# Kernel optimization log

Measured on AMD Instinct MI355X. Metric: run time of the kernel, lower is better.

Reference implementation:

```python
import jax, jax.numpy as jnp
import numpy as np

B, N, NODE_DIM = 64, 64, 192
H = 256          # node_hidden_dim
PDIM = 64        # property_embedding_dim
NUM_EDGE_TYPE = 5
T = 4            # message-passing rounds
E = 16384        # total edges (flattened batched graph)
E_SEL = 65536    # selected candidate pairs


def setup_inputs() -> dict:
    key = jax.random.key(0)
    ks = jax.random.split(key, 24)
    def g(k, shape, scale=0.05):
        return jax.random.normal(k, shape, dtype=jnp.float32) * scale
    inp = {
        "x": jax.random.normal(ks[0], (B, N, NODE_DIM), dtype=jnp.float32),
        "edge_index": jax.random.randint(ks[1], (2, E), 0, B * N, dtype=jnp.int32),
        "edge_attr": jax.random.uniform(ks[2], (E, NUM_EDGE_TYPE), dtype=jnp.float32),
        "props": jax.random.normal(ks[3], (B, 1), dtype=jnp.float32),
        "sel_b": jax.random.randint(ks[4], (E_SEL,), 0, B, dtype=jnp.int32),
        "sel_i": jax.random.randint(ks[5], (E_SEL,), 0, N, dtype=jnp.int32),
        "sel_j": jax.random.randint(ks[6], (E_SEL,), 0, N, dtype=jnp.int32),
        "golden_edge": jax.random.randint(ks[7], (E_SEL,), 0, NUM_EDGE_TYPE, dtype=jnp.int32),
        # parameters
        "W_prop": g(ks[8], (1, PDIM)), "b_prop": jnp.zeros((PDIM,), jnp.float32),
        "W_in": g(ks[9], (NODE_DIM, H)), "b_in": jnp.zeros((H,), jnp.float32),
        "W_msg": g(ks[10], (H + NUM_EDGE_TYPE, H)), "b_msg": jnp.zeros((H,), jnp.float32),
        "W_upd": g(ks[11], (2 * H, H)), "b_upd": jnp.zeros((H,), jnp.float32),
        "W_add": g(ks[12], (H + PDIM, H)), "b_add": jnp.zeros((H,), jnp.float32),
        "W1": g(ks[13], (2 * H, H)), "b1": jnp.zeros((H,), jnp.float32),
        "W2": g(ks[14], (H, H)), "b2": jnp.zeros((H,), jnp.float32),
        "W3": g(ks[15], (H, 2 * H)), "b3": jnp.zeros((2 * H,), jnp.float32),
        "W_out": g(ks[16], (2 * H, NUM_EDGE_TYPE)), "b_out": jnp.zeros((NUM_EDGE_TYPE,), jnp.float32),
    }
    return inp


def reference(x, edge_index, edge_attr, props, sel_b, sel_i, sel_j, golden_edge,
              W_prop, b_prop, W_in, b_in, W_msg, b_msg, W_upd, b_upd,
              W_add, b_add, W1, b1, W2, b2, W3, b3, W_out, b_out):
    BN = B * N
    node_x = x.reshape(BN, NODE_DIM)
    src, dst = edge_index[0], edge_index[1]

    # --- GNN node embedding (t rounds of message passing, opaque Encoder.embed_node) ---
    h = jax.nn.relu(node_x @ W_in + b_in)                       # [BN, H]
    for _ in range(T):
        msg_in = jnp.concatenate([h[src], edge_attr], axis=-1)  # [E, H+num_edge_type]
        msg = jax.nn.relu(msg_in @ W_msg + b_msg)               # [E, H]
        agg = jax.ops.segment_sum(msg, dst, num_segments=BN)    # [BN, H]
        h = jax.nn.relu(jnp.concatenate([h, agg], axis=-1) @ W_upd + b_upd)

    node_emb = h.reshape(B, N, H)

    # --- property conditioning + addition linear ---
    prop = props @ W_prop + b_prop                               # [B, PDIM]
    propp = jnp.broadcast_to(prop[:, None, :], (B, N, PDIM))
    node_embg = jnp.concatenate([node_emb, propp], axis=-1) @ W_add + b_add  # [B, N, H]

    # --- gather selected (src, dst) pairs directly (equiv. to repeat_interleave + boolean mask) ---
    flat = node_embg.reshape(BN, H)
    src_e = flat[sel_b * N + sel_i]                              # [E_SEL, H]
    dst_e = flat[sel_b * N + sel_j]                              # [E_SEL, H]
    pair = jnp.concatenate([src_e, dst_e], axis=-1)              # [E_SEL, 2H]

    # --- edge predictor MLP (3 layers, ReLU between) + output linear ---
    h1 = jax.nn.relu(pair @ W1 + b1)
    h2 = jax.nn.relu(h1 @ W2 + b2)
    h3 = h2 @ W3 + b3
    logits = h3 @ W_out + b_out                                  # [E_SEL, num_edge_type]

    # --- cross entropy (mean) ---
    logp = jax.nn.log_softmax(logits, axis=-1)
    loss = -jnp.mean(jnp.take_along_axis(logp, golden_edge[:, None].astype(jnp.int32), axis=-1))
    return loss
```

## Files before the change

kernel.cpp:

```cpp
#include <hip/hip_runtime.h>
#include <math.h>

#define BN 4096
#define N_PER_B 64
#define NE 16384
#define NSEL 65536
#define NET 5
#define PD 64
#define H1STR 260
#define FSTR 264
#define PTILES 4

typedef float f32x4 __attribute__((ext_vector_type(4)));
typedef float f32x16 __attribute__((ext_vector_type(16)));
typedef short short8 __attribute__((ext_vector_type(8)));
typedef short short4v __attribute__((ext_vector_type(4)));

__device__ __forceinline__ unsigned short f2bf(float f) {
    unsigned int u = __builtin_bit_cast(unsigned int, f);
    u += 0x7fff + ((u >> 16) & 1);
    return (unsigned short)(u >> 16);
}
__device__ __forceinline__ float bf_lo(unsigned int u) {
    return __builtin_bit_cast(float, u << 16);
}
__device__ __forceinline__ float bf_hi(unsigned int u) {
    return __builtin_bit_cast(float, u & 0xffff0000u);
}
__device__ __forceinline__ unsigned int pack2(float a, float b) {
    return (unsigned)f2bf(a) | ((unsigned)f2bf(b) << 16);
}
__device__ __forceinline__ short8 ld_frag(const unsigned short* p) {
    const short4v lo = *(const short4v*)(p);
    const short4v hi = *(const short4v*)(p + 4);
    return __builtin_shufflevector(lo, hi, 0, 1, 2, 3, 4, 5, 6, 7);
}
__device__ __forceinline__ unsigned int addrelu2(unsigned int a, unsigned int b, unsigned int c) {
    const float lo = fmaxf(bf_lo(a) + bf_lo(b) + bf_lo(c), 0.f);
    const float hi = fmaxf(bf_hi(a) + bf_hi(b) + bf_hi(c), 0.f);
    return pack2(lo, hi);
}

__global__ __launch_bounds__(256) void k_hist(const int* __restrict__ eidx,
                                              int* __restrict__ deg)
{
    const int e = blockIdx.x * 256 + threadIdx.x;
    atomicAdd(&deg[eidx[NE + e]], 1);
}

__global__ __launch_bounds__(256) void csr_scan(const int* __restrict__ deg,
                                                int* __restrict__ row_start,
                                                int* __restrict__ cursor)
{
    __shared__ int sums[256];
    const int tid = threadIdx.x;
    const int base = tid * 16;
    int local[16];
    int s = 0;
    #pragma unroll
    for (int i = 0; i < 16; ++i) { local[i] = s; s += deg[base + i]; }
    sums[tid] = s;
    __syncthreads();
    for (int off = 1; off < 256; off <<= 1) {
        const int v = sums[tid];
        const int add = (tid >= off) ? sums[tid - off] : 0;
        __syncthreads();
        sums[tid] = v + add;
        __syncthreads();
    }
    const int offset = (tid == 0) ? 0 : sums[tid - 1];
    #pragma unroll
    for (int i = 0; i < 16; ++i) {
        const int v = offset + local[i];
        row_start[base + i] = v;
        cursor[base + i] = v;
    }
    if (tid == 255) row_start[4096] = NE;
}

__global__ __launch_bounds__(256) void csr_scatter(const int* __restrict__ eidx,
                                                   int* __restrict__ cursor,
                                                   int* __restrict__ srcs,
                                                   int* __restrict__ epos)
{
    const int e = blockIdx.x * 256 + threadIdx.x;
    const int pos = atomicAdd(&cursor[eidx[NE + e]], 1);
    srcs[pos] = eidx[e];
    epos[e] = pos;
}

__global__ __launch_bounds__(256) void k_pre(
    const float* __restrict__ W_in, const float* __restrict__ W_msg,
    const float* __restrict__ W_upd, const float* __restrict__ W_add,
    const float* __restrict__ W1, const float* __restrict__ W2,
    const float* __restrict__ W3, const float* __restrict__ b3,
    const float* __restrict__ W_out, const float* __restrict__ b_out,
    const float* __restrict__ props, const float* __restrict__ W_prop,
    const float* __restrict__ b_prop, const float* __restrict__ b_add,
    const float* __restrict__ b_msg, const float* __restrict__ eattr,
    const int* __restrict__ epos,
    unsigned short* __restrict__ wbf, unsigned short* __restrict__ WfT,
    float* __restrict__ bfv, float* __restrict__ prop_add,
    unsigned short* __restrict__ ETc)
{
    __shared__ __align__(16) char smem[16704];
    const int blk = blockIdx.x;
    const int tid = threadIdx.x;

    if (blk < 128) {
        float (*s)[65] = (float(*)[65])smem;
        const int wsel = blk >> 4;
        const int sub = blk & 15;
        const float* src; unsigned short* dst; int K = 256;
        switch (wsel) {
            case 0: src = W_in;              dst = wbf;                         K = 192; break;
            case 1: src = W_msg;             dst = wbf + 49152;                 break;
            case 2: src = W_upd;             dst = wbf + 49152 + 65536;         break;
            case 3: src = W_upd + 256 * 256; dst = wbf + 49152 + 2 * 65536;     break;
            case 4: src = W_add;             dst = wbf + 49152 + 3 * 65536;     break;
            case 5: src = W1;                dst = wbf + 49152 + 4 * 65536;     break;
            case 6: src = W1 + 256 * 256;    dst = wbf + 49152 + 5 * 65536;     break;
            default: src = W2;               dst = wbf + 49152 + 6 * 65536;     break;
        }
        const int k0 = (sub >> 2) * 64;
        const int n0 = (sub & 3) * 64;
        if (k0 >= K) return;
        const int tn = tid & 63;
        const int tg = tid >> 6;
        #pragma unroll
        for (int i = 0; i < 16; ++i) {
            const int kk = tg * 16 + i;
            s[kk][tn] = src[(size_t)(k0 + kk) * 256 + n0 + tn];
        }
        __syncthreads();
        #pragma unroll
        for (int i = 0; i < 16; ++i) {
            const int nn = tg * 16 + i;
            dst[(size_t)(n0 + nn) * K + k0 + tn] = f2bf(s[tn][nn]);
        }
    } else if (blk < 192) {
        const int b = blk - 128;
        const float pv = props[b];
        float acc = b_add[tid];
        for (int p = 0; p < PD; ++p) {
            const float e = fmaf(pv, W_prop[p], b_prop[p]);
            acc = fmaf(e, W_add[(256 + p) * 256 + tid], acc);
        }
        prop_add[b * 256 + tid] = acc;
    } else if (blk < 449) {
        float* part = (float*)smem;
        const int cb = blk - 192;
        float acc[NET] = {0.f, 0.f, 0.f, 0.f, 0.f};
        #pragma unroll
        for (int rep = 0; rep < 2; ++rep) {
            const int j = rep * 256 + tid;
            const float wv = (cb < 256) ? W3[(size_t)cb * 512 + j] : b3[j];
            #pragma unroll
            for (int t = 0; t < NET; ++t) acc[t] = fmaf(wv, W_out[j * NET + t], acc[t]);
        }
        #pragma unroll
        for (int t = 0; t < NET; ++t)
            for (int off = 32; off >= 1; off >>= 1) acc[t] += __shfl_down(acc[t], off);
        if ((tid & 63) == 0) {
            #pragma unroll
            for (int t = 0; t < NET; ++t) part[(tid >> 6) * NET + t] = acc[t];
        }
        __syncthreads();
        if (tid == 0) {
            float s[NET];
            #pragma unroll
            for (int t = 0; t < NET; ++t)
                s[t] = part[t] + part[NET + t] + part[2 * NET + t] + part[3 * NET + t];
            if (cb < 256) {
                #pragma unroll
                for (int t = 0; t < NET; ++t) WfT[t * 256 + cb] = f2bf(s[t]);
                #pragma unroll
                for (int t = NET; t < 16; ++t) WfT[t * 256 + cb] = 0;
            } else {
                #pragma unroll
                for (int t = 0; t < NET; ++t) bfv[t] = s[t] + b_out[t];
            }
        }
    } else {
        float* ea = (float*)smem;
        int* eposs = (int*)(smem + 2560 + 64);
        const int eb = (blk - 449) * 128;
        if (tid < 160)
            *(float4*)&ea[tid * 4] = *(const float4*)(eattr + (size_t)eb * 5 + tid * 4);
        if (tid < 128) eposs[tid] = epos[eb + tid];
        __syncthreads();
        const float* Wme = W_msg + 256 * 256;
        const float w0 = Wme[0 * 256 + tid];
        const float w1 = Wme[1 * 256 + tid];
        const float w2 = Wme[2 * 256 + tid];
        const float w3 = Wme[3 * 256 + tid];
        const float w4 = Wme[4 * 256 + tid];
        const float bm = b_msg[tid];
        for (int i = 0; i < 128; ++i) {
            const float* a = ea + i * 5;
            float v = bm;
            v = fmaf(a[0], w0, v); v = fmaf(a[1], w1, v); v = fmaf(a[2], w2, v);
            v = fmaf(a[3], w3, v); v = fmaf(a[4], w4, v);
            ETc[(size_t)eposs[i] * 256 + tid] = f2bf(v);
        }
    }
}

__global__ __launch_bounds__(1024) void fstep(
    const float* __restrict__ x, const unsigned short* __restrict__ hbuf,
    const unsigned short* __restrict__ Pin, const unsigned short* __restrict__ ETc,
    const int* __restrict__ row_start, const int* __restrict__ srcs,
    const unsigned short* __restrict__ WaT, const unsigned short* __restrict__ WbT,
    const float* __restrict__ bias1,
    const unsigned short* __restrict__ Wp2T, const float* __restrict__ prop_add,
    const unsigned short* __restrict__ W1aT, const unsigned short* __restrict__ W1bT,
    unsigned short* __restrict__ hout, unsigned short* __restrict__ out1,
    unsigned short* __restrict__ out2, int mode)
{
    __shared__ __align__(16) unsigned short Hg[16 * FSTR];
    __shared__ __align__(16) unsigned short Ag[16 * FSTR];
    __shared__ __align__(16) unsigned short Hs[16 * FSTR];
    __shared__ __align__(16) unsigned short H2s[16 * FSTR];
    const int tid = threadIdx.x;
    const int w = tid >> 6;
    const int lane = tid & 63;
    const int q = lane >> 4;
    const int tx = lane & 15;
    const int m0 = blockIdx.x * 16;
    const int col = w * 16 + tx;

    if (mode != 0) {
        {
            const int r = tid >> 6;
            const int c4 = (tid & 63) * 4;
            *(uint2*)&Hg[r * FSTR + c4] =
                *(const uint2*)(hbuf + (size_t)(m0 + r) * 256 + c4);
        }
        {
            const int node = m0 + w;
            const int beg = row_start[node];
            const int end = row_start[node + 1];
            const int c = lane * 4;
            float a0 = 0.f, a1 = 0.f, a2 = 0.f, a3 = 0.f;
            for (int idx = beg; idx < end; ++idx) {
                const int src = srcs[idx];
                const uint2 pu = *(const uint2*)(Pin + (size_t)src * 256 + c);
                const uint2 eu = *(const uint2*)(ETc + (size_t)idx * 256 + c);
                a0 += fmaxf(bf_lo(pu.x) + bf_lo(eu.x), 0.f);
                a1 += fmaxf(bf_hi(pu.x) + bf_hi(eu.x), 0.f);
                a2 += fmaxf(bf_lo(pu.y) + bf_lo(eu.y), 0.f);
                a3 += fmaxf(bf_hi(pu.y) + bf_hi(eu.y), 0.f);
            }
            uint2 o; o.x = pack2(a0, a1); o.y = pack2(a2, a3);
            *(uint2*)&Ag[w * FSTR + c] = o;
        }
        __syncthreads();
    }

    f32x4 acc = (f32x4)0.f;
    if (mode == 0) {
        #pragma unroll
        for (int s = 0; s < 6; ++s) {
            const int k0 = s * 32;
            const float* ap = x + (size_t)(m0 + tx) * 192 + k0 + q * 8;
            const float4 v0 = *(const float4*)ap;
            const float4 v1 = *(const float4*)(ap + 4);
            short8 af;
            af[0] = (short)f2bf(v0.x); af[1] = (short)f2bf(v0.y);
            af[2] = (short)f2bf(v0.z); af[3] = (short)f2bf(v0.w);
            af[4] = (short)f2bf(v1.x); af[5] = (short)f2bf(v1.y);
            af[6] = (short)f2bf(v1.z); af[7] = (short)f2bf(v1.w);
            const short8 bfr = *(const short8*)(WaT + (size_t)col * 192 + k0 + q * 8);
            acc = __builtin_amdgcn_mfma_f32_16x16x32_bf16(af, bfr, acc, 0, 0, 0);
        }
    } else {
        #pragma unroll
        for (int s = 0; s < 8; ++s) {
            const int k0 = s * 32;
            const short8 af = *(const short8*)&Hg[tx * FSTR + k0 + q * 8];
            const short8 bfr = *(const short8*)(WaT + (size_t)col * 256 + k0 + q * 8);
            acc = __builtin_amdgcn_mfma_f32_16x16x32_bf16(af, bfr, acc, 0, 0, 0);
        }
        #pragma unroll
        for (int s = 0; s < 8; ++s) {
            const int k0 = s * 32;
            const short8 af = *(const short8*)&Ag[tx * FSTR + k0 + q * 8];
            const short8 bfr = *(const short8*)(WbT + (size_t)col * 256 + k0 + q * 8);
            acc = __builtin_amdgcn_mfma_f32_16x16x32_bf16(af, bfr, acc, 0, 0, 0);
        }
    }
    {
        const float bv = bias1[col];
        #pragma unroll
        for (int r = 0; r < 4; ++r) {
            const int row = q * 4 + r;
            const unsigned short us = f2bf(fmaxf(acc[r] + bv, 0.f));
            Hs[row * FSTR + col] = us;
            if (mode < 2) hout[(size_t)(m0 + row) * 256 + col] = us;
        }
    }
    __syncthreads();

    acc = (f32x4)0.f;
    #pragma unroll
    for (int s = 0; s < 8; ++s) {
        const int k0 = s * 32;
        const short8 af = *(const short8*)&Hs[tx * FSTR + k0 + q * 8];
        const short8 bfr = *(const short8*)(Wp2T + (size_t)col * 256 + k0 + q * 8);
        acc = __builtin_amdgcn_mfma_f32_16x16x32_bf16(af, bfr, acc, 0, 0, 0);
    }
    if (mode < 2) {
        #pragma unroll
        for (int r = 0; r < 4; ++r)
            out1[(size_t)(m0 + q * 4 + r) * 256 + col] = f2bf(acc[r]);
        return;
    }
    {
        const float pv = prop_add[(m0 >> 6) * 256 + col];
        #pragma unroll
        for (int r = 0; r < 4; ++r)
            H2s[(q * 4 + r) * FSTR + col] = f2bf(acc[r] + pv);
    }
    __syncthreads();

    for (int which = 0; which < 2; ++which) {
        const unsigned short* WT = which ? W1bT : W1aT;
        unsigned short* op = which ? out2 : out1;
        acc = (f32x4)0.f;
        #pragma unroll
        for (int s = 0; s < 8; ++s) {
            const int k0 = s * 32;
            const short8 af = *(const short8*)&H2s[tx * FSTR + k0 + q * 8];
            const short8 bfr = *(const short8*)(WT + (size_t)col * 256 + k0 + q * 8);
            acc = __builtin_amdgcn_mfma_f32_16x16x32_bf16(af, bfr, acc, 0, 0, 0);
        }
        #pragma unroll
        for (int r = 0; r < 4; ++r)
            op[(size_t)(m0 + q * 4 + r) * 256 + col] = f2bf(acc[r]);
    }
}

__global__ __launch_bounds__(512, 1) void pair_k(
    const unsigned short* __restrict__ A1t, const unsigned short* __restrict__ A2t,
    const float* __restrict__ b1, const unsigned short* __restrict__ W2T,
    const float* __restrict__ b2, const unsigned short* __restrict__ WfT,
    const float* __restrict__ bfv,
    const int* __restrict__ sel_b, const int* __restrict__ sel_i,
    const int* __restrict__ sel_j, const int* __restrict__ golden,
    float* __restrict__ out)
{
    __shared__ __align__(16) unsigned short sbuf[64 * H1STR];
    __shared__ __align__(16) unsigned short b1s[256];
    __shared__ float Lg[64 * 8];
    __shared__ int sidx[64 * PTILES], didx[64 * PTILES], gold[64 * PTILES];

    const int tid = threadIdx.x;
    const int w = tid >> 6;
    const int lane = tid & 63;
    const int q = lane >> 4;
    const int tx = lane & 15;
    const int m = lane & 31;
    const int hh = lane >> 5;
    const int e0 = blockIdx.x * 64 * PTILES;

    if (tid < 64 * PTILES) {
        const int e = e0 + tid;
        const int b = sel_b[e];
        sidx[tid] = b * N_PER_B + sel_i[e];
        didx[tid] = b * N_PER_B + sel_j[e];
        gold[tid] = golden[e];
    }
    if (tid < 256) b1s[tid] = f2bf(b1[tid]);

    const int pt = w & 1;
    const int cg = w >> 1;
    short8 Breg[32];
    {
        const unsigned short* bb = W2T + (size_t)(cg * 64 + m) * 256 + hh * 8;
        #pragma unroll
        for (int cc = 0; cc < 2; ++cc)
            #pragma unroll
            for (int s = 0; s < 16; ++s)
                Breg[cc * 16 + s] = *(const short8*)(bb + (size_t)cc * 32 * 256 + s * 16);
    }
    __syncthreads();

    float total = 0.f;

    for (int t = 0; t < PTILES; ++t) {
        {
            const int hw = tid >> 5;
            #pragma unroll
            for (int j = 0; j < 4; ++j) {
                const int p = j * 16 + hw;
                const unsigned short* r1 = A1t + (size_t)sidx[t * 64 + p] * 256 + m * 8;
                const unsigned short* r2 = A2t + (size_t)didx[t * 64 + p] * 256 + m * 8;
                const uint4 u1 = *(const uint4*)r1;
                const uint4 u2 = *(const uint4*)r2;
                const uint4 ub = *(const uint4*)(b1s + m * 8);
                uint2 lo2, hi2;
                lo2.x = addrelu2(u1.x, u2.x, ub.x);
                lo2.y = addrelu2(u1.y, u2.y, ub.y);
                hi2.x = addrelu2(u1.z, u2.z, ub.z);
                hi2.y = addrelu2(u1.w, u2.w, ub.w);
                unsigned short* dbase = sbuf + p * H1STR + m * 8;
                *(uint2*)(dbase) = lo2;
                *(uint2*)(dbase + 4) = hi2;
            }
        }
        __syncthreads();

        f32x16 acc0 = (f32x16)0.f;
        f32x16 acc1 = (f32x16)0.f;
        {
            const unsigned short* arow = sbuf + (size_t)(pt * 32 + m) * H1STR + hh * 8;
            #pragma unroll
            for (int s = 0; s < 16; ++s) {
                const short8 af = ld_frag(arow + s * 16);
                acc0 = __builtin_amdgcn_mfma_f32_32x32x16_bf16(af, Breg[s], acc0, 0, 0, 0);
                acc1 = __builtin_amdgcn_mfma_f32_32x32x16_bf16(af, Breg[16 + s], acc1, 0, 0, 0);
            }
        }
        __syncthreads();

        #pragma unroll
        for (int cc = 0; cc < 2; ++cc) {
            const f32x16* ap = cc ? &acc1 : &acc0;
            const int col = cg * 64 + cc * 32 + m;
            const float bv = b2[col];
            #pragma unroll
            for (int reg = 0; reg < 16; ++reg) {
                const int prow = pt * 32 + (reg & 3) + 8 * (reg >> 2) + 4 * hh;
                sbuf[prow * H1STR + col] = f2bf(fmaxf((*ap)[reg] + bv, 0.f));
            }
        }
        __syncthreads();

        if (w < 4) {
            f32x4 accL = (f32x4)0.f;
            const unsigned short* a2row = sbuf + (size_t)(w * 16 + tx) * H1STR + q * 8;
            const unsigned short* bWf = WfT + (size_t)tx * 256 + q * 8;
            #pragma unroll
            for (int s = 0; s < 8; ++s) {
                const short8 af = ld_frag(a2row + s * 32);
                const short8 bfr = *(const short8*)(bWf + s * 32);
                accL = __builtin_amdgcn_mfma_f32_16x16x32_bf16(af, bfr, accL, 0, 0, 0);
            }
            if (tx < NET) {
                const float bb = bfv[tx];
                #pragma unroll
                for (int reg = 0; reg < 4; ++reg)
                    Lg[(w * 16 + q * 4 + reg) * 8 + tx] = accL[reg] + bb;
            }
        }
        __syncthreads();

        if (tid < 64) {
            float lg[NET];
            #pragma unroll
            for (int tt = 0; tt < NET; ++tt) lg[tt] = Lg[tid * 8 + tt];
            float mx = lg[0];
            #pragma unroll
            for (int tt = 1; tt < NET; ++tt) mx = fmaxf(mx, lg[tt]);
            float s = 0.f;
            #pragma unroll
            for (int tt = 0; tt < NET; ++tt) s += expf(lg[tt] - mx);
            float ls = mx + logf(s) - lg[gold[t * 64 + tid]];
            #pragma unroll
            for (int off = 32; off >= 1; off >>= 1) ls += __shfl_xor(ls, off);
            total += ls;
        }
        __syncthreads();
    }

    if (tid == 0) atomicAdd(out, total * (1.0f / NSEL));
}

extern "C" void kernel_launch(void* const* d_in, const int* in_sizes, int n_in,
                              void* d_out, int out_size, void* d_ws, size_t ws_size,
                              hipStream_t stream) {
    (void)in_sizes; (void)n_in; (void)out_size; (void)ws_size;
    const float* x      = (const float*)d_in[0];
    const int*   eidx   = (const int*)d_in[1];
    const float* eattr  = (const float*)d_in[2];
    const float* props  = (const float*)d_in[3];
    const int*   sel_b  = (const int*)d_in[4];
    const int*   sel_i  = (const int*)d_in[5];
    const int*   sel_j  = (const int*)d_in[6];
    const int*   golden = (const int*)d_in[7];
    const float* W_prop = (const float*)d_in[8];
    const float* b_prop = (const float*)d_in[9];
    const float* W_in   = (const float*)d_in[10];
    const float* b_in   = (const float*)d_in[11];
    const float* W_msg  = (const float*)d_in[12];
    const float* b_msg  = (const float*)d_in[13];
    const float* W_upd  = (const float*)d_in[14];
    const float* b_upd  = (const float*)d_in[15];
    const float* W_add  = (const float*)d_in[16];
    const float* b_add  = (const float*)d_in[17];
    const float* W1     = (const float*)d_in[18];
    const float* b1     = (const float*)d_in[19];
    const float* W2     = (const float*)d_in[20];
    const float* b2     = (const float*)d_in[21];
    const float* W3     = (const float*)d_in[22];
    const float* b3     = (const float*)d_in[23];
    const float* W_out  = (const float*)d_in[24];
    const float* b_out  = (const float*)d_in[25];

    const size_t SEG = (size_t)BN * 256;
    unsigned short* P0   = (unsigned short*)d_ws;
    unsigned short* P1   = P0 + SEG;
    unsigned short* hA   = P1 + SEG;
    unsigned short* hB   = hA + SEG;
    unsigned short* ETc  = hB + SEG;
    unsigned short* wbf  = ETc + (size_t)NE * 256;
    unsigned short* W_inT  = wbf;
    unsigned short* WmT    = wbf + 49152;
    unsigned short* WuaT   = WmT + 65536;
    unsigned short* WubT   = WuaT + 65536;
    unsigned short* W_addT = WubT + 65536;
    unsigned short* W1aT   = W_addT + 65536;
    unsigned short* W1bT   = W1aT + 65536;
    unsigned short* W2T    = W1bT + 65536;
    unsigned short* WfT    = W2T + 65536;
    float* prop_add = (float*)(WfT + 4096);
    float* bfv = prop_add + 64 * 256;
    int* deg       = (int*)(bfv + 16);
    int* row_start = deg + 4096;
    int* cursor    = row_start + 4104;
    int* srcs      = cursor + 4096;
    int* epos      = srcs + NE;

    hipMemsetAsync(deg, 0, 4096 * sizeof(int), stream);
    k_hist<<<NE / 256, 256, 0, stream>>>(eidx, deg);
    csr_scan<<<1, 256, 0, stream>>>(deg, row_start, cursor);
    csr_scatter<<<NE / 256, 256, 0, stream>>>(eidx, cursor, srcs, epos);
    k_pre<<<577, 256, 0, stream>>>(W_in, W_msg, W_upd, W_add, W1, W2, W3, b3,
                                   W_out, b_out, props, W_prop, b_prop, b_add,
                                   b_msg, eattr, epos, wbf, WfT, bfv, prop_add, ETc);

    fstep<<<256, 1024, 0, stream>>>(x, nullptr, nullptr, ETc, row_start, srcs,
                                    W_inT, nullptr, b_in, WmT, nullptr, nullptr, nullptr,
                                    hA, P0, nullptr, 0);
    fstep<<<256, 1024, 0, stream>>>(nullptr, hA, P0, ETc, row_start, srcs,
                                    WuaT, WubT, b_upd, WmT, nullptr, nullptr, nullptr,
                                    hB, P1, nullptr, 1);
    fstep<<<256, 1024, 0, stream>>>(nullptr, hB, P1, ETc, row_start, srcs,
                                    WuaT, WubT, b_upd, WmT, nullptr, nullptr, nullptr,
                                    hA, P0, nullptr, 1);
    fstep<<<256, 1024, 0, stream>>>(nullptr, hA, P0, ETc, row_start, srcs,
                                    WuaT, WubT, b_upd, WmT, nullptr, nullptr, nullptr,
                                    hB, P1, nullptr, 1);
    fstep<<<256, 1024, 0, stream>>>(nullptr, hB, P1, ETc, row_start, srcs,
                                    WuaT, WubT, b_upd, W_addT, prop_add, W1aT, W1bT,
                                    nullptr, P0, hA, 2);

    hipMemsetAsync(d_out, 0, sizeof(float), stream);
    pair_k<<<256, 512, 0, stream>>>(P0, hA, b1, W2T, b2, WfT, bfv,
                                    sel_b, sel_i, sel_j, golden, (float*)d_out);
}
```

Baseline: 252.4 us.

## Fuse message-passing rounds into one cooperative kernel with grid barriers

The five per-round fstep launches become a single cooperative kernel, mp_all. It uses a hand-rolled atomic grid barrier between rounds and keeps each block's node hidden state in shared memory, so it no longer goes through global memory. This removes four kernel-launch gaps and the global writes and reads of h. The cost is the spin-barrier overhead. The barrier also has a guard timeout, which could let execution run ahead unsafely if it fires.

```diff
diff --git a/kernel.cpp b/kernel.cpp
--- a/kernel.cpp
+++ b/kernel.cpp
@@ -41,6 +41,21 @@
     return pack2(lo, hi);
 }
 
+__device__ __forceinline__ void gsync(int* bar, int target) {
+    __builtin_amdgcn_fence(__ATOMIC_RELEASE, "agent");
+    __syncthreads();
+    if (threadIdx.x == 0) {
+        __hip_atomic_fetch_add(bar, 1, __ATOMIC_RELAXED, __HIP_MEMORY_SCOPE_AGENT);
+        int guard = 0;
+        while (__hip_atomic_load(bar, __ATOMIC_RELAXED, __HIP_MEMORY_SCOPE_AGENT) < target) {
+            if (++guard >= (1 << 18)) break;
+            __builtin_amdgcn_s_sleep(8);
+        }
+    }
+    __syncthreads();
+    __builtin_amdgcn_fence(__ATOMIC_ACQUIRE, "agent");
+}
+
 __global__ __launch_bounds__(256) void k_hist(const int* __restrict__ eidx,
                                               int* __restrict__ deg)
 {
@@ -50,7 +65,8 @@
 
 __global__ __launch_bounds__(256) void csr_scan(const int* __restrict__ deg,
                                                 int* __restrict__ row_start,
-                                                int* __restrict__ cursor)
+                                                int* __restrict__ cursor,
+                                                int* __restrict__ bar)
 {
     __shared__ int sums[256];
     const int tid = threadIdx.x;
@@ -76,6 +92,7 @@
         cursor[base + i] = v;
     }
     if (tid == 255) row_start[4096] = NE;
+    if (tid == 0) *bar = 0;
 }
 
 __global__ __launch_bounds__(256) void csr_scatter(const int* __restrict__ eidx,
@@ -206,21 +223,24 @@
     }
 }
 
-__global__ __launch_bounds__(1024) void fstep(
-    const float* __restrict__ x, const unsigned short* __restrict__ hbuf,
-    const unsigned short* __restrict__ Pin, const unsigned short* __restrict__ ETc,
+__global__ __launch_bounds__(1024, 4) void mp_all(
+    const float* __restrict__ x, const unsigned short* __restrict__ ETc,
     const int* __restrict__ row_start, const int* __restrict__ srcs,
-    const unsigned short* __restrict__ WaT, const unsigned short* __restrict__ WbT,
-    const float* __restrict__ bias1,
-    const unsigned short* __restrict__ Wp2T, const float* __restrict__ prop_add,
+    const unsigned short* __restrict__ W_inT, const unsigned short* __restrict__ WmT,
+    const unsigned short* __restrict__ WuaT, const unsigned short* __restrict__ WubT,
+    const unsigned short* __restrict__ W_addT,
     const unsigned short* __restrict__ W1aT, const unsigned short* __restrict__ W1bT,
-    unsigned short* __restrict__ hout, unsigned short* __restrict__ out1,
-    unsigned short* __restrict__ out2, int mode)
+    const float* __restrict__ b_in, const float* __restrict__ b_upd,
+    const float* __restrict__ prop_add,
+    unsigned short* __restrict__ P0g, unsigned short* __restrict__ P1g,
+    unsigned short* __restrict__ A2g,
+    int* __restrict__ bar)
 {
-    __shared__ __align__(16) unsigned short Hg[16 * FSTR];
+    __shared__ __align__(16) unsigned short Ha[16 * FSTR];
+    __shared__ __align__(16) unsigned short Hb[16 * FSTR];
     __shared__ __align__(16) unsigned short Ag[16 * FSTR];
-    __shared__ __align__(16) unsigned short Hs[16 * FSTR];
     __shared__ __align__(16) unsigned short H2s[16 * FSTR];
+
     const int tid = threadIdx.x;
     const int w = tid >> 6;
     const int lane = tid & 63;
@@ -229,13 +249,52 @@
     const int m0 = blockIdx.x * 16;
     const int col = w * 16 + tx;
 
-    if (mode != 0) {
-        {
-            const int r = tid >> 6;
-            const int c4 = (tid & 63) * 4;
-            *(uint2*)&Hg[r * FSTR + c4] =
-                *(const uint2*)(hbuf + (size_t)(m0 + r) * 256 + c4);
-        }
+    {
+        f32x4 acc = (f32x4)0.f;
+        #pragma unroll
+        for (int s = 0; s < 6; ++s) {
+            const int k0 = s * 32;
+            const float* ap = x + (size_t)(m0 + tx) * 192 + k0 + q * 8;
+            const float4 v0 = *(const float4*)ap;
+            const float4 v1 = *(const float4*)(ap + 4);
+            short8 af;
+            af[0] = (short)f2bf(v0.x); af[1] = (short)f2bf(v0.y);
+            af[2] = (short)f2bf(v0.z); af[3] = (short)f2bf(v0.w);
+            af[4] = (short)f2bf(v1.x); af[5] = (short)f2bf(v1.y);
+            af[6] = (short)f2bf(v1.z); af[7] = (short)f2bf(v1.w);
+            const short8 bfr = *(const short8*)(W_inT + (size_t)col * 192 + k0 + q * 8);
+            acc = __builtin_amdgcn_mfma_f32_16x16x32_bf16(af, bfr, acc, 0, 0, 0);
+        }
+        const float bv = b_in[col];
+        #pragma unroll
+        for (int r = 0; r < 4; ++r)
+            Ha[(q * 4 + r) * FSTR + col] = f2bf(fmaxf(acc[r] + bv, 0.f));
+    }
+    __syncthreads();
+    {
+        f32x4 acc = (f32x4)0.f;
+        const unsigned short* hrow = Ha + tx * FSTR;
+        const unsigned short* bcol = WmT + (size_t)col * 256;
+        #pragma unroll
+        for (int s = 0; s < 8; ++s) {
+            const int k0 = s * 32;
+            const short8 af = *(const short8*)(hrow + k0 + q * 8);
+            const short8 bfr = *(const short8*)(bcol + k0 + q * 8);
+            acc = __builtin_amdgcn_mfma_f32_16x16x32_bf16(af, bfr, acc, 0, 0, 0);
+        }
+        #pragma unroll
+        for (int r = 0; r < 4; ++r)
+            P0g[(size_t)(m0 + q * 4 + r) * 256 + col] = f2bf(acc[r]);
+    }
+    gsync(bar, 256);
+
+    #pragma unroll
+    for (int t = 1; t <= 3; ++t) {
+        const unsigned short* Pin = (t & 1) ? P0g : P1g;
+        unsigned short* Pout      = (t & 1) ? P1g : P0g;
+        const unsigned short* Hc  = (t & 1) ? Ha : Hb;
+        unsigned short* Hn        = (t & 1) ? Hb : Ha;
+
         {
             const int node = m0 + w;
             const int beg = row_start[node];
@@ -255,67 +314,110 @@
             *(uint2*)&Ag[w * FSTR + c] = o;
         }
         __syncthreads();
-    }
-
-    f32x4 acc = (f32x4)0.f;
-    if (mode == 0) {
-        #pragma unroll
-        for (int s = 0; s < 6; ++s) {
-            const int k0 = s * 32;
-            const float* ap = x + (size_t)(m0 + tx) * 192 + k0 + q * 8;
-            const float4 v0 = *(const float4*)ap;
-            const float4 v1 = *(const float4*)(ap + 4);
-            short8 af;
-            af[0] = (short)f2bf(v0.x); af[1] = (short)f2bf(v0.y);
-            af[2] = (short)f2bf(v0.z); af[3] = (short)f2bf(v0.w);
-            af[4] = (short)f2bf(v1.x); af[5] = (short)f2bf(v1.y);
-            af[6] = (short)f2bf(v1.z); af[7] = (short)f2bf(v1.w);
-            const short8 bfr = *(const short8*)(WaT + (size_t)col * 192 + k0 + q * 8);
-            acc = __builtin_amdgcn_mfma_f32_16x16x32_bf16(af, bfr, acc, 0, 0, 0);
-        }
-    } else {
+
+        {
+            f32x4 acc = (f32x4)0.f;
+            const unsigned short* hrow = Hc + tx * FSTR;
+            const unsigned short* arow = Ag + tx * FSTR;
+            const unsigned short* bca = WuaT + (size_t)col * 256;
+            const unsigned short* bcb = WubT + (size_t)col * 256;
+            #pragma unroll
+            for (int s = 0; s < 8; ++s) {
+                const int k0 = s * 32;
+                const short8 af = *(const short8*)(hrow + k0 + q * 8);
+                const short8 bfr = *(const short8*)(bca + k0 + q * 8);
+                acc = __builtin_amdgcn_mfma_f32_16x16x32_bf16(af, bfr, acc, 0, 0, 0);
+            }
+            #pragma unroll
+            for (int s = 0; s < 8; ++s) {
+                const int k0 = s * 32;
+                const short8 af = *(const short8*)(arow + k0 + q * 8);
+                const short8 bfr = *(const short8*)(bcb + k0 + q * 8);
+                acc = __builtin_amdgcn_mfma_f32_16x16x32_bf16(af, bfr, acc, 0, 0, 0);
+            }
+            const float bv = b_upd[col];
+            #pragma unroll
+            for (int r = 0; r < 4; ++r)
+                Hn[(q * 4 + r) * FSTR + col] = f2bf(fmaxf(acc[r] + bv, 0.f));
+        }
+        __syncthreads();
+
+        {
+            f32x4 acc = (f32x4)0.f;
+            const unsigned short* hrow = Hn + tx * FSTR;
+            const unsigned short* bcol = WmT + (size_t)col * 256;
+            #pragma unroll
+            for (int s = 0; s < 8; ++s) {
+                const int k0 = s * 32;
+                const short8 af = *(const short8*)(hrow + k0 + q * 8);
+                const short8 bfr = *(const short8*)(bcol + k0 + q * 8);
+                acc = __builtin_amdgcn_mfma_f32_16x16x32_bf16(af, bfr, acc, 0, 0, 0);
+            }
+            #pragma unroll
+            for (int r = 0; r < 4; ++r)
+                Pout[(size_t)(m0 + q * 4 + r) * 256 + col] = f2bf(acc[r]);
+        }
+        gsync(bar, 256 * (t + 1));
+    }
+
+    {
+        const int node = m0 + w;
+        const int beg = row_start[node];
+        const int end = row_start[node + 1];
+        const int c = lane * 4;
+        float a0 = 0.f, a1 = 0.f, a2 = 0.f, a3 = 0.f;
+        for (int idx = beg; idx < end; ++idx) {
+            const int src = srcs[idx];
+            const uint2 pu = *(const uint2*)(P1g + (size_t)src * 256 + c);
+            const uint2 eu = *(const uint2*)(ETc + (size_t)idx * 256 + c);
+            a0 += fmaxf(bf_lo(pu.x) + bf_lo(eu.x), 0.f);
+            a1 += fmaxf(bf_hi(pu.x) + bf_hi(eu.x), 0.f);
+            a2 += fmaxf(bf_lo(pu.y) + bf_lo(eu.y), 0.f);
+            a3 += fmaxf(bf_hi(pu.y) + bf_hi(eu.y), 0.f);
+        }
+        uint2 o; o.x = pack2(a0, a1); o.y = pack2(a2, a3);
+        *(uint2*)&Ag[w * FSTR + c] = o;
+    }
+    __syncthreads();
+
+    {
+        f32x4 acc = (f32x4)0.f;
+        const unsigned short* hrow = Hb + tx * FSTR;
+        const unsigned short* arow = Ag + tx * FSTR;
+        const unsigned short* bca = WuaT + (size_t)col * 256;
+        const unsigned short* bcb = WubT + (size_t)col * 256;
         #pragma unroll
         for (int s = 0; s < 8; ++s) {
             const int k0 = s * 32;
-            const short8 af = *(const short8*)&Hg[tx * FSTR + k0 + q * 8];
-            const short8 bfr = *(const short8*)(WaT + (size_t)col * 256 + k0 + q * 8);
+            const short8 af = *(const short8*)(hrow + k0 + q * 8);
+            const short8 bfr = *(const short8*)(bca + k0 + q * 8);
             acc = __builtin_amdgcn_mfma_f32_16x16x32_bf16(af, bfr, acc, 0, 0, 0);
         }
         #pragma unroll
         for (int s = 0; s < 8; ++s) {
             const int k0 = s * 32;
-            const short8 af = *(const short8*)&Ag[tx * FSTR + k0 + q * 8];
-            const short8 bfr = *(const short8*)(WbT + (size_t)col * 256 + k0 + q * 8);
+            const short8 af = *(const short8*)(arow + k0 + q * 8);
+            const short8 bfr = *(const short8*)(bcb + k0 + q * 8);
             acc = __builtin_amdgcn_mfma_f32_16x16x32_bf16(af, bfr, acc, 0, 0, 0);
         }
-    }
+        const float bv = b_upd[col];
+        #pragma unroll
+        for (int r = 0; r < 4; ++r)
+            Ha[(q * 4 + r) * FSTR + col] = f2bf(fmaxf(acc[r] + bv, 0.f));
+    }
+    __syncthreads();
+
     {
-        const float bv = bias1[col];
-        #pragma unroll
-        for (int r = 0; r < 4; ++r) {
-            const int row = q * 4 + r;
-            const unsigned short us = f2bf(fmaxf(acc[r] + bv, 0.f));
-            Hs[row * FSTR + col] = us;
-            if (mode < 2) hout[(size_t)(m0 + row) * 256 + col] = us;
-        }
-    }
-    __syncthreads();
-
-    acc = (f32x4)0.f;
-    #pragma unroll
-    for (int s = 0; s < 8; ++s) {
-        const int k0 = s * 32;
-        const short8 af = *(const short8*)&Hs[tx * FSTR + k0 + q * 8];
-        const short8 bfr = *(const short8*)(Wp2T + (size_t)col * 256 + k0 + q * 8);
-        acc = __builtin_amdgcn_mfma_f32_16x16x32_bf16(af, bfr, acc, 0, 0, 0);
-    }
-    if (mode < 2) {
-        #pragma unroll
-        for (int r = 0; r < 4; ++r)
-            out1[(size_t)(m0 + q * 4 + r) * 256 + col] = f2bf(acc[r]);
-        return;
-    }
-    {
+        f32x4 acc = (f32x4)0.f;
+        const unsigned short* hrow = Ha + tx * FSTR;
+        const unsigned short* bcol = W_addT + (size_t)col * 256;
+        #pragma unroll
+        for (int s = 0; s < 8; ++s) {
+            const int k0 = s * 32;
+            const short8 af = *(const short8*)(hrow + k0 + q * 8);
+            const short8 bfr = *(const short8*)(bcol + k0 + q * 8);
+            acc = __builtin_amdgcn_mfma_f32_16x16x32_bf16(af, bfr, acc, 0, 0, 0);
+        }
         const float pv = prop_add[(m0 >> 6) * 256 + col];
         #pragma unroll
         for (int r = 0; r < 4; ++r)
@@ -323,15 +425,18 @@
     }
     __syncthreads();
 
+    #pragma unroll
     for (int which = 0; which < 2; ++which) {
         const unsigned short* WT = which ? W1bT : W1aT;
-        unsigned short* op = which ? out2 : out1;
-        acc = (f32x4)0.f;
+        unsigned short* op = which ? A2g : P0g;
+        f32x4 acc = (f32x4)0.f;
+        const unsigned short* hrow = H2s + tx * FSTR;
+        const unsigned short* bcol = WT + (size_t)col * 256;
         #pragma unroll
         for (int s = 0; s < 8; ++s) {
             const int k0 = s * 32;
-            const short8 af = *(const short8*)&H2s[tx * FSTR + k0 + q * 8];
-            const short8 bfr = *(const short8*)(WT + (size_t)col * 256 + k0 + q * 8);
+            const short8 af = *(const short8*)(hrow + k0 + q * 8);
+            const short8 bfr = *(const short8*)(bcol + k0 + q * 8);
             acc = __builtin_amdgcn_mfma_f32_16x16x32_bf16(af, bfr, acc, 0, 0, 0);
         }
         #pragma unroll
@@ -530,30 +635,27 @@
     int* cursor    = row_start + 4104;
     int* srcs      = cursor + 4096;
     int* epos      = srcs + NE;
+    int* bar       = epos + NE;
 
     hipMemsetAsync(deg, 0, 4096 * sizeof(int), stream);
     k_hist<<<NE / 256, 256, 0, stream>>>(eidx, deg);
-    csr_scan<<<1, 256, 0, stream>>>(deg, row_start, cursor);
+    csr_scan<<<1, 256, 0, stream>>>(deg, row_start, cursor, bar);
     csr_scatter<<<NE / 256, 256, 0, stream>>>(eidx, cursor, srcs, epos);
     k_pre<<<577, 256, 0, stream>>>(W_in, W_msg, W_upd, W_add, W1, W2, W3, b3,
                                    W_out, b_out, props, W_prop, b_prop, b_add,
                                    b_msg, eattr, epos, wbf, WfT, bfv, prop_add, ETc);
 
-    fstep<<<256, 1024, 0, stream>>>(x, nullptr, nullptr, ETc, row_start, srcs,
-                                    W_inT, nullptr, b_in, WmT, nullptr, nullptr, nullptr,
-                                    hA, P0, nullptr, 0);
-    fstep<<<256, 1024, 0, stream>>>(nullptr, hA, P0, ETc, row_start, srcs,
-                                    WuaT, WubT, b_upd, WmT, nullptr, nullptr, nullptr,
-                                    hB, P1, nullptr, 1);
-    fstep<<<256, 1024, 0, stream>>>(nullptr, hB, P1, ETc, row_start, srcs,
-                                    WuaT, WubT, b_upd, WmT, nullptr, nullptr, nullptr,
-                                    hA, P0, nullptr, 1);
-    fstep<<<256, 1024, 0, stream>>>(nullptr, hA, P0, ETc, row_start, srcs,
-                                    WuaT, WubT, b_upd, WmT, nullptr, nullptr, nullptr,
-                                    hB, P1, nullptr, 1);
-    fstep<<<256, 1024, 0, stream>>>(nullptr, hB, P1, ETc, row_start, srcs,
-                                    WuaT, WubT, b_upd, W_addT, prop_add, W1aT, W1bT,
-                                    nullptr, P0, hA, 2);
+    {
+        void* args[] = {
+            (void*)&x, (void*)&ETc, (void*)&row_start, (void*)&srcs,
+            (void*)&W_inT, (void*)&WmT, (void*)&WuaT, (void*)&WubT,
+            (void*)&W_addT, (void*)&W1aT, (void*)&W1bT,
+            (void*)&b_in, (void*)&b_upd, (void*)&prop_add,
+            (void*)&P0, (void*)&P1, (void*)&hA, (void*)&bar
+        };
+        hipLaunchCooperativeKernel((const void*)mp_all, dim3(256), dim3(1024),
+                                   args, 0, stream);
+    }
 
     hipMemsetAsync(d_out, 0, sizeof(float), stream);
     pair_k<<<256, 512, 0, stream>>>(P0, hA, b1, W2T, b2, WfT, bfv,
```

After: 791.4 us. +213.6%, slower.

## Halve pair tiles per block and remap W2 fragments for two blocks per CU

Applied to the files above, without the earlier changes.

In the pair kernel each wave now holds a 32-column slice of W2 (16 register fragments instead of 32) and computes both 32-row halves of the 64-pair tile, where before it held two column slices for one row half. Fewer weight registers let the launch bound allow two blocks per CU. PTILES drops from 4 to 2, so the grid doubles to 512 blocks. The aim is more resident waves to hide gather and LDS latency. The cost is twice the W2 register loading per pair processed and more atomic partial sums.

```diff
diff --git a/kernel.cpp b/kernel.cpp
--- a/kernel.cpp
+++ b/kernel.cpp
@@ -9,7 +9,7 @@
 #define PD 64
 #define H1STR 260
 #define FSTR 264
-#define PTILES 4
+#define PTILES 2
 
 typedef float f32x4 __attribute__((ext_vector_type(4)));
 typedef float f32x16 __attribute__((ext_vector_type(16)));
@@ -340,7 +340,7 @@
     }
 }
 
-__global__ __launch_bounds__(512, 1) void pair_k(
+__global__ __launch_bounds__(512, 2) void pair_k(
     const unsigned short* __restrict__ A1t, const unsigned short* __restrict__ A2t,
     const float* __restrict__ b1, const unsigned short* __restrict__ W2T,
     const float* __restrict__ b2, const unsigned short* __restrict__ WfT,
@@ -372,16 +372,12 @@
     }
     if (tid < 256) b1s[tid] = f2bf(b1[tid]);
 
-    const int pt = w & 1;
-    const int cg = w >> 1;
-    short8 Breg[32];
+    short8 Breg[16];
     {
-        const unsigned short* bb = W2T + (size_t)(cg * 64 + m) * 256 + hh * 8;
-        #pragma unroll
-        for (int cc = 0; cc < 2; ++cc)
-            #pragma unroll
-            for (int s = 0; s < 16; ++s)
-                Breg[cc * 16 + s] = *(const short8*)(bb + (size_t)cc * 32 * 256 + s * 16);
+        const unsigned short* bb = W2T + (size_t)(w * 32 + m) * 256 + hh * 8;
+        #pragma unroll
+        for (int s = 0; s < 16; ++s)
+            Breg[s] = *(const short8*)(bb + s * 16);
     }
     __syncthreads();
 
@@ -413,25 +409,26 @@
         f32x16 acc0 = (f32x16)0.f;
         f32x16 acc1 = (f32x16)0.f;
         {
-            const unsigned short* arow = sbuf + (size_t)(pt * 32 + m) * H1STR + hh * 8;
+            const unsigned short* a0row = sbuf + (size_t)m * H1STR + hh * 8;
+            const unsigned short* a1row = a0row + 32 * H1STR;
             #pragma unroll
             for (int s = 0; s < 16; ++s) {
-                const short8 af = ld_frag(arow + s * 16);
-                acc0 = __builtin_amdgcn_mfma_f32_32x32x16_bf16(af, Breg[s], acc0, 0, 0, 0);
-                acc1 = __builtin_amdgcn_mfma_f32_32x32x16_bf16(af, Breg[16 + s], acc1, 0, 0, 0);
-            }
-        }
-        __syncthreads();
-
-        #pragma unroll
-        for (int cc = 0; cc < 2; ++cc) {
-            const f32x16* ap = cc ? &acc1 : &acc0;
-            const int col = cg * 64 + cc * 32 + m;
+                const short8 af0 = ld_frag(a0row + s * 16);
+                acc0 = __builtin_amdgcn_mfma_f32_32x32x16_bf16(af0, Breg[s], acc0, 0, 0, 0);
+                const short8 af1 = ld_frag(a1row + s * 16);
+                acc1 = __builtin_amdgcn_mfma_f32_32x32x16_bf16(af1, Breg[s], acc1, 0, 0, 0);
+            }
+        }
+        __syncthreads();
+
+        {
+            const int col = w * 32 + m;
             const float bv = b2[col];
             #pragma unroll
             for (int reg = 0; reg < 16; ++reg) {
-                const int prow = pt * 32 + (reg & 3) + 8 * (reg >> 2) + 4 * hh;
-                sbuf[prow * H1STR + col] = f2bf(fmaxf((*ap)[reg] + bv, 0.f));
+                const int prow = (reg & 3) + 8 * (reg >> 2) + 4 * hh;
+                sbuf[prow * H1STR + col] = f2bf(fmaxf(acc0[reg] + bv, 0.f));
+                sbuf[(32 + prow) * H1STR + col] = f2bf(fmaxf(acc1[reg] + bv, 0.f));
             }
         }
         __syncthreads();
@@ -556,6 +553,6 @@
                                     nullptr, P0, hA, 2);
 
     hipMemsetAsync(d_out, 0, sizeof(float), stream);
-    pair_k<<<256, 512, 0, stream>>>(P0, hA, b1, W2T, b2, WfT, bfv,
+    pair_k<<<NSEL / (64 * PTILES), 512, 0, stream>>>(P0, hA, b1, W2T, b2, WfT, bfv,
                                     sel_b, sel_i, sel_j, golden, (float*)d_out);
 }
```

After: 254.2 us. No clear change (+0.7%).
